# Optimization experiments

Measured on AMD Instinct MI355X. Metric: run time of the kernel, lower is better.

## Reference

```python
import jax, jax.numpy as jnp
import numpy as np

B, N, M, C, K = 4, 16384, 1024, 256, 32
RADIUS = 1.0
EPS = 1e-5


def _bn(x, g, b, axes):
    # training-mode batch norm over given axes; channel axis is 1
    m = jnp.mean(x, axes, keepdims=True)
    v = jnp.var(x, axes, keepdims=True)
    sh = [1] * x.ndim
    sh[1] = -1
    return (x - m) * jax.lax.rsqrt(v + EPS) * g.reshape(sh) + b.reshape(sh)


def setup_inputs() -> dict:
    key = jax.random.key(0)
    ks = jax.random.split(key, 10)
    d = {
        'ffps_xyz': jax.random.normal(ks[0], (B, M, 3), jnp.float32),
        'ffps_feature': jax.random.normal(ks[1], (B, C, M), jnp.float32),
        'backbone_xyz': jax.random.normal(ks[2], (B, N, 3), jnp.float32),
        'backbone_features': jax.random.normal(ks[3], (B, C, N), jnp.float32),
        # shift layer: Conv1d(256->128), Conv1d(128->3)
        'sw1': jax.random.normal(ks[4], (128, 256), jnp.float32) * 0.05,
        'sg1': jnp.ones((128,), jnp.float32), 'sb1': jnp.zeros((128,), jnp.float32),
        'sw2': jax.random.normal(ks[5], (3, 128), jnp.float32) * 0.05,
        'sg2': jnp.ones((3,), jnp.float32), 'sb2': jnp.zeros((3,), jnp.float32),
        # grouped MLP: Conv2d 1x1: 259->512->512->512
        'w1': jax.random.normal(ks[6], (512, C + 3), jnp.float32) * 0.05,
        'g1': jnp.ones((512,), jnp.float32), 'b1': jnp.zeros((512,), jnp.float32),
        'w2': jax.random.normal(ks[7], (512, 512), jnp.float32) * 0.05,
        'g2': jnp.ones((512,), jnp.float32), 'b2': jnp.zeros((512,), jnp.float32),
        'w3': jax.random.normal(ks[8], (512, 512), jnp.float32) * 0.05,
        'g3': jnp.ones((512,), jnp.float32), 'b3': jnp.zeros((512,), jnp.float32),
    }
    return d


def reference(ffps_xyz, ffps_feature, backbone_xyz, backbone_features,
              sw1, sg1, sb1, sw2, sg2, sb2,
              w1, g1, b1, w2, g2, b2, w3, g3, b3):
    # ---- shift layer: Conv1d(1x1)+BN1d+ReLU x2 -> (B,3,M) ----
    h = jnp.einsum('oc,bcm->bom', sw1, ffps_feature)
    h = jax.nn.relu(_bn(h, sg1, sb1, (0, 2)))
    h = jnp.einsum('oc,bcm->bom', sw2, h)
    shift = jax.nn.relu(_bn(h, sg2, sb2, (0, 2)))
    new_xyz = ffps_xyz + shift.transpose(0, 2, 1)  # (B,M,3)

    # ---- ball query: first K points within RADIUS, pad with first hit ----
    d2 = jnp.sum((new_xyz[:, :, None, :] - backbone_xyz[:, None, :, :]) ** 2, -1)  # (B,M,N)
    score = jnp.where(d2 < RADIUS * RADIUS, jnp.arange(N, dtype=jnp.int32), N)
    neg_vals, _ = jax.lax.top_k(-score, K)  # K smallest scores = first valid indices
    idx = -neg_vals  # (B,M,K)
    first = idx[..., :1]
    idx = jnp.where(idx == N, first, idx)
    idx = jnp.where(idx == N, 0, idx)  # query with no neighbors -> 0

    # ---- group: relative xyz concat features -> (B, 3+C, M, K) ----
    bidx = jnp.arange(B)[:, None, None]
    g_xyz = backbone_xyz[bidx, idx] - new_xyz[:, :, None, :]        # (B,M,K,3)
    g_feat = backbone_features.transpose(0, 2, 1)[bidx, idx]        # (B,M,K,C)
    g = jnp.concatenate([g_xyz, g_feat], -1).transpose(0, 3, 1, 2)  # (B,3+C,M,K)

    # ---- per-point MLP: Conv2d(1x1)+BN2d+ReLU x3 ----
    for w, gm, bt in ((w1, g1, b1), (w2, g2, b2), (w3, g3, b3)):
        g = jnp.einsum('oc,bcmk->bomk', w, g)
        g = jax.nn.relu(_bn(g, gm, bt, (0, 2, 3)))

    # ---- max-pool over neighbors, return (B, M, C_out) ----
    return jnp.max(g, axis=3).transpose(0, 2, 1)
```

## Files before the change

### kernel.cpp

```cpp
#include <hip/hip_runtime.h>
#include <hip/hip_bf16.h>
#include <hip/hip_fp16.h>

#define BB   4
#define NN   16384
#define MM   1024
#define CC   256
#define KK   32
#define O1   128
#define FF   512
#define LTOT (BB*MM*KK)
#define NSLOT 64
#define CH   16384
#define NCH2 (LTOT/CH)

typedef float f4 __attribute__((ext_vector_type(4)));
typedef short b8 __attribute__((ext_vector_type(8)));

__device__ __forceinline__ float bf2f(unsigned short u){
    return __uint_as_float(((unsigned int)u) << 16);
}
__device__ __forceinline__ float anyf(const void* p, size_t i, int f){
    if (f == 1) return bf2f(((const unsigned short*)p)[i]);
    if (f == 2) return __half2float(((const __half*)p)[i]);
    return ((const float*)p)[i];
}

__global__ void k_det(const unsigned short* __restrict__ u, int n, int* __restrict__ flag){
    if (threadIdx.x != 0 || blockIdx.x != 0) return;
    int W = n < 64 ? n : 64;
    bool allz = true;
    for (int k = 0; k < W; k++) if (u[k]){ allz = false; break; }
    if (allz){ *flag = 1; return; }
    if (u[0] == 0x3F80u){ *flag = 1; return; }
    if (u[0] == 0x3C00u){ *flag = 2; return; }
    if (W >= 2){
        unsigned int f0 = ((unsigned int)u[1] << 16) | u[0];
        if (__uint_as_float(f0) == 1.0f){ *flag = 0; return; }
    }
    int ce = 0, co = 0, ne = 0, no_ = 0;
    for (int k = 0; k < W; k++){
        unsigned short x = u[k];
        float v = fabsf(bf2f(x));
        int sane = (x == 0) || (v >= 0.0009765625f && v <= 64.f);
        if (k & 1){ no_++; co += sane; } else { ne++; ce += sane; }
    }
    if (ce * 4 >= ne * 3){ *flag = 1; return; }
    if (co * 4 >= no_ * 3 && ce * 5 < ne * 2){ *flag = 0; return; }
    *flag = 2;
}

__global__ __launch_bounds__(256) void k_cvtf(const void* __restrict__ src,
                                              float* __restrict__ dst, int n,
                                              const int* __restrict__ flag){
    int t = blockIdx.x * 256 + threadIdx.x;
    if (t >= n) return;
    dst[t] = anyf(src, t, *flag);
}

__global__ __launch_bounds__(256) void k_mlp1(const float* __restrict__ sw1,
                                              const float* __restrict__ feat,
                                              float* __restrict__ h1,
                                              float* __restrict__ stats1){
    int t = blockIdx.x * 256 + threadIdx.x;
    int m = t & (MM - 1);
    int o = (t >> 10) & (O1 - 1);
    int b = t >> 17;
    const float* fb = feat + (size_t)b * CC * MM + m;
    const float* w  = sw1 + o * CC;
    float acc = 0.f;
    #pragma unroll 8
    for (int c = 0; c < CC; c++) acc += w[c] * fb[(size_t)c * MM];
    h1[t] = acc;
    float s = acc, s2 = acc * acc;
    for (int off = 32; off; off >>= 1){ s += __shfl_down(s, off); s2 += __shfl_down(s2, off); }
    __shared__ float ls[8];
    int lane = threadIdx.x & 63, wid = threadIdx.x >> 6;
    if (lane == 0){ ls[wid] = s; ls[4 + wid] = s2; }
    __syncthreads();
    if (threadIdx.x == 0){
        atomicAdd(&stats1[2*o],   ls[0]+ls[1]+ls[2]+ls[3]);
        atomicAdd(&stats1[2*o+1], ls[4]+ls[5]+ls[6]+ls[7]);
    }
}

__global__ __launch_bounds__(256) void k_bn1mlp2(const float* __restrict__ h1,
                                                 const float* __restrict__ stats1,
                                                 const float* __restrict__ sg1,
                                                 const float* __restrict__ sb1,
                                                 const float* __restrict__ sw2,
                                                 float* __restrict__ h2,
                                                 float* __restrict__ stats2){
    __shared__ float sc[O1], bi[O1];
    int tid = threadIdx.x;
    if (tid < O1){
        const float invn = 1.f / (BB * MM);
        float mean = stats1[2*tid] * invn;
        float var  = fmaxf(stats1[2*tid+1] * invn - mean * mean, 0.f);
        float rs   = 1.f / sqrtf(var + 1e-5f);
        float s    = rs * sg1[tid];
        float b_   = sb1[tid] - mean * s;
        if (!isfinite(s) || !isfinite(b_)){ s = 1.f; b_ = 0.f; }
        sc[tid] = s; bi[tid] = b_;
    }
    __syncthreads();
    int t = blockIdx.x * 256 + tid;
    int m = t & (MM - 1);
    int r = t >> 10; int o2 = r % 3; int b = r / 3;
    const float* hb = h1 + (size_t)b * O1 * MM + m;
    const float* w  = sw2 + o2 * O1;
    float acc = 0.f;
    #pragma unroll 8
    for (int c = 0; c < O1; c++){
        float v = hb[(size_t)c * MM] * sc[c] + bi[c];
        v = v > 0.f ? v : 0.f;
        acc += w[c] * v;
    }
    h2[t] = acc;
    float s = acc, s2 = acc * acc;
    for (int off = 32; off; off >>= 1){ s += __shfl_down(s, off); s2 += __shfl_down(s2, off); }
    __shared__ float ls[8];
    int lane = tid & 63, wid = tid >> 6;
    if (lane == 0){ ls[wid] = s; ls[4 + wid] = s2; }
    __syncthreads();
    if (tid == 0){
        atomicAdd(&stats2[2*o2],   ls[0]+ls[1]+ls[2]+ls[3]);
        atomicAdd(&stats2[2*o2+1], ls[4]+ls[5]+ls[6]+ls[7]);
    }
}

__global__ void k_fin2(const float* __restrict__ stats2, const float* __restrict__ sg2,
                       const float* __restrict__ sb2, float* __restrict__ scb2){
    int t = threadIdx.x;
    if (t < 3){
        const float invn = 1.f / (BB * MM);
        float mean = stats2[2*t] * invn;
        float var  = fmaxf(stats2[2*t+1] * invn - mean * mean, 0.f);
        float rs   = 1.f / sqrtf(var + 1e-5f);
        float s    = rs * sg2[t];
        float b    = sb2[t] - mean * s;
        if (!isfinite(s) || !isfinite(b)){ s = 1.f; b = 0.f; }
        scb2[t] = s; scb2[4 + t] = b;
    }
}

__global__ __launch_bounds__(256) void k_ballq(const float* __restrict__ fxyz,
                                               const float* __restrict__ h2,
                                               const float* __restrict__ scb2,
                                               const float* __restrict__ bxyz,
                                               float* __restrict__ nxyz,
                                               int* __restrict__ idxbuf){
    int q    = blockIdx.x * 4 + (threadIdx.x >> 6);
    int lane = threadIdx.x & 63;
    int b = q >> 10, m = q & (MM - 1);
    float nx[3];
    #pragma unroll
    for (int c = 0; c < 3; c++){
        float v = h2[((size_t)b * 3 + c) * MM + m] * scb2[c] + scb2[4 + c];
        v = v > 0.f ? v : 0.f;
        nx[c] = fxyz[(size_t)q * 3 + c] + v;
    }
    if (lane == 0){
        nxyz[q*3+0] = nx[0]; nxyz[q*3+1] = nx[1]; nxyz[q*3+2] = nx[2];
    }
    const float* bx = bxyz + (size_t)b * NN * 3;
    int have = 0, firstj = 0;
    int* out = idxbuf + (size_t)q * KK;
    for (int j0 = 0; j0 < NN && have < KK; j0 += 64){
        int j = j0 + lane;
        float dx = bx[j*3+0] - nx[0];
        float dy = bx[j*3+1] - nx[1];
        float dz = bx[j*3+2] - nx[2];
        float d2 = dx*dx + dy*dy + dz*dz;
        bool pred = d2 < 1.0f;
        unsigned long long mask = __ballot(pred);
        if (mask){
            if (have == 0) firstj = j0 + (__ffsll((unsigned long long)mask) - 1);
            if (pred){
                int rank = __popcll(mask & ((1ull << lane) - 1ull));
                int pos = have + rank;
                if (pos < KK) out[pos] = j;
            }
            have += (int)__popcll(mask);
        }
    }
    if (have < KK){
        int fill = (have > 0) ? firstj : 0;
        for (int p = have + lane; p < KK; p += 64) out[p] = fill;
    }
}

__global__ __launch_bounds__(256) void k_xyzd(const int* __restrict__ idxbuf,
                                              const float* __restrict__ bxyz,
                                              const float* __restrict__ nxyz,
                                              int* __restrict__ idx2,
                                              float4* __restrict__ xyzd){
    int l = blockIdx.x * 256 + threadIdx.x;
    int b = l >> 15;
    int q = l >> 5;
    int j = idxbuf[l];
    idx2[l] = b * NN + j;
    const float* p = bxyz + ((size_t)b * NN + j) * 3;
    xyzd[l] = make_float4(p[0] - nxyz[q*3+0], p[1] - nxyz[q*3+1], p[2] - nxyz[q*3+2], 0.f);
}

__global__ __launch_bounds__(256) void k_transp(const void* __restrict__ bfv,
                                                const int* __restrict__ flag,
                                                float* __restrict__ ft){
    __shared__ float tile[32][33];
    int f = *flag;
    int bid = blockIdx.x;
    int nt = bid & 511;
    int ct = (bid >> 9) & 7;
    int b  = bid >> 12;
    int tx = threadIdx.x & 31, ty = threadIdx.x >> 5;
    size_t base = ((size_t)b * CC + ct * 32) * NN + nt * 32;
    #pragma unroll
    for (int r = 0; r < 32; r += 8)
        tile[ty + r][tx] = anyf(bfv, base + (size_t)(ty + r) * NN + tx, f);
    __syncthreads();
    float* dst = ft + ((size_t)b * NN + nt * 32) * CC + ct * 32;
    #pragma unroll
    for (int r = 0; r < 32; r += 8) dst[(size_t)(ty + r) * CC + tx] = tile[tx][ty + r];
}

__global__ void k_wprep(const float* __restrict__ w1,
                        unsigned short* __restrict__ w1h,
                        unsigned short* __restrict__ w1l,
                        float4* __restrict__ w1xp){
    int t = blockIdx.x * 256 + threadIdx.x;
    int o = t >> 8, c = t & 255;
    float f = w1[o * 259 + 3 + c];
    unsigned u = __float_as_uint(f);
    unsigned hh = u & 0xFFFF0000u;
    w1h[t] = (unsigned short)(hh >> 16);
    float f2 = f - __uint_as_float(hh);
    w1l[t] = (unsigned short)(__float_as_uint(f2) >> 16);
    if (t < 512) w1xp[t] = make_float4(w1[t*259], w1[t*259+1], w1[t*259+2], 0.f);
}

__global__ __launch_bounds__(256) void k_wsplit(const float* __restrict__ src,
                                                unsigned short* __restrict__ h,
                                                unsigned short* __restrict__ l, int n){
    int t = blockIdx.x * 256 + threadIdx.x;
    if (t >= n) return;
    float f = src[t];
    unsigned u = __float_as_uint(f);
    unsigned hh = u & 0xFFFF0000u;
    h[t] = (unsigned short)(hh >> 16);
    float f2 = f - __uint_as_float(hh);
    l[t] = (unsigned short)(__float_as_uint(f2) >> 16);
}

__device__ __forceinline__ void split4(float x, float y, float z_, float w_,
                                       unsigned &h0, unsigned &h1,
                                       unsigned &lo0, unsigned &lo1){
    unsigned ux = __float_as_uint(x), uy = __float_as_uint(y);
    unsigned uz = __float_as_uint(z_), uw = __float_as_uint(w_);
    unsigned hx = ux & 0xFFFF0000u, hy = uy & 0xFFFF0000u;
    unsigned hz = uz & 0xFFFF0000u, hw = uw & 0xFFFF0000u;
    h0 = (hx >> 16) | hy;
    h1 = (hz >> 16) | hw;
    float rx = x  - __uint_as_float(hx);
    float ry = y  - __uint_as_float(hy);
    float rz = z_ - __uint_as_float(hz);
    float rw = w_ - __uint_as_float(hw);
    lo0 = (__float_as_uint(rx) >> 16) | (__float_as_uint(ry) & 0xFFFF0000u);
    lo1 = (__float_as_uint(rz) >> 16) | (__float_as_uint(rw) & 0xFFFF0000u);
}

template<int XM, int OM>
__global__ __launch_bounds__(256) void k_gemm(const unsigned short* __restrict__ Ah,
                                              const unsigned short* __restrict__ Al,
                                              const float* __restrict__ X,
                                              int Cs,
                                              const float* __restrict__ scb,
                                              const int* __restrict__ idx2,
                                              const float4* __restrict__ xyzd,
                                              const float4* __restrict__ w1xp,
                                              int Lbase,
                                              float* __restrict__ Y,
                                              int Lwrite,
                                              float* __restrict__ y3mx,
                                              float* __restrict__ y3mn,
                                              double* __restrict__ stats){
    __shared__ short lds[16384];
    char* ldsb = (char*)lds;

    const int tid  = threadIdx.x;
    const int lane = tid & 63;
    const int w    = tid >> 6;
    const int wo   = (w >> 1) * 64;
    const int wl   = (w & 1) * 64;

    int bid = blockIdx.x;
    {
        int cpx = gridDim.x >> 3;
        bid = (bid & 7) * cpx + (bid >> 3);
    }
    const int o0 = (bid & 3) * 128;
    const int l0 = (bid >> 2) * 128;

    const int o_loc  = tid >> 3;
    const int q      = (tid & 7) >> 1;
    const int h      = tid & 1;
    const int colOff = q * 8 + h * 4;
    const int wbase  = ((o_loc >> 4) * 1024) + (((o_loc & 15) * 16) ^ (q << 5)) + (q << 8) + h * 8;
    const int roff   = (((lane & 15) * 16) ^ ((lane >> 4) << 5)) + ((lane >> 4) << 8);

    const unsigned short* Ahp = Ah + (size_t)(o0 + o_loc) * Cs + colOff;
    const unsigned short* Alp = Al + (size_t)(o0 + o_loc) * Cs + colOff;

    int   rI[4];
    float ddx[4], ddy[4], ddz[4];
    const float* Xp = nullptr;
    if (XM == 1){
        #pragma unroll
        for (int i = 0; i < 4; i++){
            int lg = Lbase + l0 + o_loc + 32 * i;
            rI[i] = idx2[lg];
            float4 dd = xyzd[lg];
            ddx[i] = dd.x; ddy[i] = dd.y; ddz[i] = dd.z;
        }
    } else {
        Xp = X + (size_t)(l0 + o_loc) * Cs + colOff;
    }

    f4 acc[4][4];
    #pragma unroll
    for (int i = 0; i < 4; i++)
        #pragma unroll
        for (int j = 0; j < 4; j++)
            acc[i][j] = f4{0.f, 0.f, 0.f, 0.f};

    uint2  rah[4], ral[4];
    float4 rx[4];
    #pragma unroll
    for (int i = 0; i < 4; i++){
        rah[i] = *(const uint2*)(Ahp + (size_t)(32 * i) * Cs);
        ral[i] = *(const uint2*)(Alp + (size_t)(32 * i) * Cs);
        if (XM == 1) rx[i] = *(const float4*)(X + (size_t)rI[i] * FF + colOff);
        else         rx[i] = *(const float4*)(Xp + (size_t)(32 * i) * Cs);
    }

    for (int c0 = 0; c0 < Cs; c0 += 32){
        unsigned xh0[4], xh1[4], xL0[4], xL1[4];
        float4 sc4, bi4;
        if (scb){
            sc4 = *(const float4*)(scb + c0 + colOff);
            bi4 = *(const float4*)(scb + Cs + c0 + colOff);
        }
        float4 wv0, wv1, wv2, wv3;
        if (XM == 1){
            wv0 = w1xp[c0 + colOff + 0];
            wv1 = w1xp[c0 + colOff + 1];
            wv2 = w1xp[c0 + colOff + 2];
            wv3 = w1xp[c0 + colOff + 3];
        }
        #pragma unroll
        for (int i = 0; i < 4; i++){
            float vx = rx[i].x, vy = rx[i].y, vz = rx[i].z, vw = rx[i].w;
            if (XM == 1){
                vx += ddx[i]*wv0.x + ddy[i]*wv0.y + ddz[i]*wv0.z;
                vy += ddx[i]*wv1.x + ddy[i]*wv1.y + ddz[i]*wv1.z;
                vz += ddx[i]*wv2.x + ddy[i]*wv2.y + ddz[i]*wv2.z;
                vw += ddx[i]*wv3.x + ddy[i]*wv3.y + ddz[i]*wv3.z;
            }
            if (scb){
                vx = fmaxf(vx * sc4.x + bi4.x, 0.f);
                vy = fmaxf(vy * sc4.y + bi4.y, 0.f);
                vz = fmaxf(vz * sc4.z + bi4.z, 0.f);
                vw = fmaxf(vw * sc4.w + bi4.w, 0.f);
            }
            split4(vx, vy, vz, vw, xh0[i], xh1[i], xL0[i], xL1[i]);
        }
        __syncthreads();
        #pragma unroll
        for (int i = 0; i < 4; i++){
            int off = wbase + i * 2048;
            *(uint2*)(ldsb + off)          = rah[i];
            *(uint2*)(ldsb + 8192  + off)  = ral[i];
            *(uint2*)(ldsb + 16384 + off)  = make_uint2(xh0[i], xh1[i]);
            *(uint2*)(ldsb + 24576 + off)  = make_uint2(xL0[i], xL1[i]);
        }
        __syncthreads();
        if (c0 + 32 < Cs){
            #pragma unroll
            for (int i = 0; i < 4; i++){
                rah[i] = *(const uint2*)(Ahp + (size_t)(32 * i) * Cs + (c0 + 32));
                ral[i] = *(const uint2*)(Alp + (size_t)(32 * i) * Cs + (c0 + 32));
                if (XM == 1) rx[i] = *(const float4*)(X + (size_t)rI[i] * FF + colOff + (c0 + 32));
                else         rx[i] = *(const float4*)(Xp + (size_t)(32 * i) * Cs + (c0 + 32));
            }
        }
        b8 bhf[4], blf[4];
        #pragma unroll
        for (int ni = 0; ni < 4; ni++){
            int f = (wl >> 4) + ni;
            bhf[ni] = *(const b8*)(ldsb + 16384 + f * 1024 + roff);
            blf[ni] = *(const b8*)(ldsb + 24576 + f * 1024 + roff);
        }
        #pragma unroll
        for (int mi = 0; mi < 4; mi++){
            int f = (wo >> 4) + mi;
            b8 ahf = *(const b8*)(ldsb + f * 1024 + roff);
            b8 alf = *(const b8*)(ldsb + 8192 + f * 1024 + roff);
            #pragma unroll
            for (int ni = 0; ni < 4; ni++){
                acc[mi][ni] = __builtin_amdgcn_mfma_f32_16x16x32_bf16(ahf, bhf[ni], acc[mi][ni], 0, 0, 0);
                acc[mi][ni] = __builtin_amdgcn_mfma_f32_16x16x32_bf16(ahf, blf[ni], acc[mi][ni], 0, 0, 0);
                acc[mi][ni] = __builtin_amdgcn_mfma_f32_16x16x32_bf16(alf, bhf[ni], acc[mi][ni], 0, 0, 0);
            }
        }
    }

    if (OM == 0){
        if (Y && (l0 + 128 <= Lwrite)){
            #pragma unroll
            for (int mi = 0; mi < 4; mi++){
                #pragma unroll
                for (int ni = 0; ni < 4; ni++){
                    int o = o0 + wo + mi * 16 + 4 * (lane >> 4);
                    int l = l0 + wl + ni * 16 + (lane & 15);
                    *(float4*)(Y + (size_t)l * FF + o) =
                        make_float4(acc[mi][ni][0], acc[mi][ni][1], acc[mi][ni][2], acc[mi][ni][3]);
                }
            }
        }
    }
    if (stats){
        int slot_s = blockIdx.x & (NSLOT - 1);
        double* sp = stats + (size_t)slot_s * FF * 2;
        #pragma unroll
        for (int mi = 0; mi < 4; mi++){
            float s1[4] = {0,0,0,0}, s2[4] = {0,0,0,0};
            #pragma unroll
            for (int ni = 0; ni < 4; ni++){
                #pragma unroll
                for (int r = 0; r < 4; r++){
                    float v = acc[mi][ni][r];
                    s1[r] += v; s2[r] += v * v;
                }
            }
            #pragma unroll
            for (int off = 8; off; off >>= 1){
                #pragma unroll
                for (int r = 0; r < 4; r++){
                    s1[r] += __shfl_down(s1[r], off, 16);
                    s2[r] += __shfl_down(s2[r], off, 16);
                }
            }
            if ((lane & 15) == 0){
                int o = o0 + wo + mi * 16 + 4 * (lane >> 4);
                #pragma unroll
                for (int r = 0; r < 4; r++){
                    atomicAdd(&sp[2 * (o + r)],     (double)s1[r]);
                    atomicAdd(&sp[2 * (o + r) + 1], (double)s2[r]);
                }
            }
        }
    }
    if (OM == 1){
        #pragma unroll
        for (int mi = 0; mi < 4; mi++){
            #pragma unroll
            for (int g = 0; g < 2; g++){
                float vmx[4], vmn[4];
                #pragma unroll
                for (int r = 0; r < 4; r++){
                    float a0 = acc[mi][2*g][r], a1 = acc[mi][2*g+1][r];
                    vmx[r] = fmaxf(a0, a1); vmn[r] = fminf(a0, a1);
                }
                #pragma unroll
                for (int off = 8; off; off >>= 1){
                    #pragma unroll
                    for (int r = 0; r < 4; r++){
                        vmx[r] = fmaxf(vmx[r], __shfl_down(vmx[r], off, 16));
                        vmn[r] = fminf(vmn[r], __shfl_down(vmn[r], off, 16));
                    }
                }
                if ((lane & 15) == 0){
                    int qg = (Lbase + l0 + wl) / 32 + g;
                    #pragma unroll
                    for (int r = 0; r < 4; r++){
                        int o = o0 + wo + mi * 16 + 4 * (lane >> 4) + r;
                        y3mx[(size_t)qg * FF + o] = vmx[r];
                        y3mn[(size_t)qg * FF + o] = vmn[r];
                    }
                }
            }
        }
    }
}

__global__ void k_finL(const double* __restrict__ stats, const float* __restrict__ g,
                       const float* __restrict__ bt, float* __restrict__ scb){
    int o = blockIdx.x * 256 + threadIdx.x;
    double s = 0.0, s2 = 0.0;
    for (int k = 0; k < NSLOT; k++){
        s  += stats[((size_t)k * FF + o) * 2];
        s2 += stats[((size_t)k * FF + o) * 2 + 1];
    }
    double mean = s / (double)LTOT;
    double var  = s2 / (double)LTOT - mean * mean;
    if (!(var > 0.0)) var = 0.0;
    double rs = 1.0 / sqrt(var + 1e-5);
    double sc = rs * (double)g[o];
    double bi = (double)bt[o] - mean * sc;
    float scf = (float)sc, bif = (float)bi;
    if (!isfinite(scf) || !isfinite(bif)){ scf = 1.f; bif = 0.f; }
    scb[o] = scf;
    scb[FF + o] = bif;
}

__global__ __launch_bounds__(256) void k_y1stats(const float* __restrict__ z,
                                                 const int* __restrict__ idx2,
                                                 const float4* __restrict__ xyzd,
                                                 const float4* __restrict__ w1xp,
                                                 double* __restrict__ stats){
    int tid = threadIdx.x, bid = blockIdx.x;
    int o1 = tid, o2 = tid + 256;
    float4 wa = w1xp[o1], wb = w1xp[o2];
    double s1a=0, s2a=0, s1b=0, s2b=0;
    for (int p = 0; p < LTOT/2048; p++){
        int l = bid + p * 2048;
        int r = idx2[l];
        float4 d = xyzd[l];
        const float* zr = z + (size_t)r * FF;
        float ya = zr[o1] + d.x*wa.x + d.y*wa.y + d.z*wa.z;
        float yb = zr[o2] + d.x*wb.x + d.y*wb.y + d.z*wb.z;
        s1a += ya; s2a += (double)ya*ya;
        s1b += yb; s2b += (double)yb*yb;
    }
    int slot = bid & (NSLOT - 1);
    double* sp = stats + (size_t)slot * FF * 2;
    atomicAdd(&sp[2*o1],   s1a); atomicAdd(&sp[2*o1+1], s2a);
    atomicAdd(&sp[2*o2],   s1b); atomicAdd(&sp[2*o2+1], s2b);
}

__global__ __launch_bounds__(256) void k_bn3max(const float* __restrict__ mx,
                                                const float* __restrict__ mn,
                                                const float* __restrict__ scb,
                                                float* __restrict__ out){
    int t = blockIdx.x * 256 + threadIdx.x;
    int o = t & (FF - 1);
    float sc = scb[o], bi = scb[FF + o];
    float v = sc >= 0.f ? mx[t] : mn[t];
    out[t] = fmaxf(sc * v + bi, 0.f);
}

__global__ __launch_bounds__(256) void k_diag(const float* __restrict__ ff,
                                              const float* __restrict__ w1f,
                                              const float* __restrict__ featT,
                                              const float* __restrict__ z,
                                              const float* __restrict__ xyzdf,
                                              const float* __restrict__ scb1,
                                              const float* __restrict__ scbL2,
                                              const float* __restrict__ scbL3,
                                              const float* __restrict__ y3,
                                              float* __restrict__ out){
    __shared__ float red[4];
    int tid = threadIdx.x;
    int bad = 0, isn = 0;
    const float* arr[9] = {ff, w1f, featT, z, xyzdf, scb1, scbL2, scbL3, y3};
    const int   len[9] = {4096, 4096, 8192, 8192, 4096, 1024, 1024, 1024, 8192};
    for (int k = 0; k < 9; k++){
        float s = 0.f;
        const float* a = arr[k];
        for (int i = tid; i < len[k]; i += 256) s += fabsf(a[i]);
        for (int off = 32; off; off >>= 1) s += __shfl_down(s, off);
        if ((tid & 63) == 0) red[tid >> 6] = s;
        __syncthreads();
        float t = red[0] + red[1] + red[2] + red[3];
        __syncthreads();
        if (bad == 0 && !(t > 1e-6f && t < 1e15f)){
            bad = k + 1;
            isn = isfinite(t) ? 0 : 1;
        }
    }
    if (tid == 0 && bad) out[0] = 512.f * bad + 256.f * isn;
}

extern "C" void kernel_launch(void* const* d_in, const int* in_sizes, int n_in,
                              void* d_out, int out_size, void* d_ws, size_t ws_size,
                              hipStream_t stream) {
    static const int NSZ[19] = {12288, 1048576, 196608, 16777216, 32768, 128, 128,
                                384, 3, 3, 132608, 512, 512, 262144, 512, 512,
                                262144, 512, 512};
    float* out = (float*)d_out;

    char* w = (char*)d_ws;
    size_t off = 0;
    auto take = [&](size_t bytes)->size_t{
        size_t r = off; off += (bytes + 255) & ~(size_t)255; return r;
    };
    size_t o_stats1  = take(256 * 4);
    size_t o_stats2  = take(8 * 4);
    size_t o_statsA  = take((size_t)NSLOT * FF * 2 * 8);
    size_t o_statsL2 = take((size_t)NSLOT * FF * 2 * 8);
    size_t o_statsL3 = take((size_t)NSLOT * FF * 2 * 8);
    size_t zero_end  = off;
    size_t o_flags   = take(19 * 4);
    size_t o_cv[19];
    for (int i = 0; i < 19; i++){
        if (i == 3){ o_cv[i] = 0; continue; }
        o_cv[i] = take((size_t)NSZ[i] * 4);
    }
    size_t o_scb2    = take(8 * 4);
    size_t o_scb1    = take(FF * 2 * 4);
    size_t o_scbL2   = take(FF * 2 * 4);
    size_t o_scbL3   = take(FF * 2 * 4);
    size_t o_h1      = take((size_t)BB * O1 * MM * 4);
    size_t o_h2      = take((size_t)BB * 3 * MM * 4);
    size_t o_nxyz    = take((size_t)BB * MM * 3 * 4);
    size_t o_idx     = take((size_t)LTOT * 4);
    size_t o_idx2    = take((size_t)LTOT * 4);
    size_t o_xyzd    = take((size_t)LTOT * 16);
    size_t o_w1h     = take((size_t)FF * CC * 2);
    size_t o_w1l     = take((size_t)FF * CC * 2);
    size_t o_w2h     = take((size_t)FF * FF * 2);
    size_t o_w2l     = take((size_t)FF * FF * 2);
    size_t o_w3h     = take((size_t)FF * FF * 2);
    size_t o_w3l     = take((size_t)FF * FF * 2);
    size_t o_w1xp    = take((size_t)FF * 16);
    size_t o_y3mx    = take((size_t)BB * MM * FF * 4);
    size_t o_y3mn    = take((size_t)BB * MM * FF * 4);
    size_t o_z       = take((size_t)BB * NN * FF * 4);
    size_t o_featT   = take((size_t)BB * NN * CC * 4);
    (void)n_in; (void)in_sizes; (void)out_size;

    const size_t chb = (size_t)CH * FF * 4;
    size_t avail = ws_size > o_featT ? ws_size - o_featT : 0;
    int S; bool full;
    if (avail >= (size_t)NCH2 * chb){ S = NCH2; full = true; }
    else {
        long s = (long)(avail / chb) - 1;
        if (s < 0) s = 0; if (s > NCH2 - 1) s = NCH2 - 1;
        S = (int)s; full = false;
    }
    const int Lwrite = S * CH;

    float*  stats1  = (float*) (w + o_stats1);
    float*  stats2  = (float*) (w + o_stats2);
    double* statsA  = (double*)(w + o_statsA);
    double* statsL2 = (double*)(w + o_statsL2);
    double* statsL3 = (double*)(w + o_statsL3);
    int*    flags   = (int*)   (w + o_flags);
    float*  scb2    = (float*) (w + o_scb2);
    float*  scb1    = (float*) (w + o_scb1);
    float*  scbL2   = (float*) (w + o_scbL2);
    float*  scbL3   = (float*) (w + o_scbL3);
    float*  h1      = (float*) (w + o_h1);
    float*  h2      = (float*) (w + o_h2);
    float*  nxyz    = (float*) (w + o_nxyz);
    int*    idxbuf  = (int*)   (w + o_idx);
    int*    idx2    = (int*)   (w + o_idx2);
    float4* xyzd    = (float4*)(w + o_xyzd);
    unsigned short* w1h = (unsigned short*)(w + o_w1h);
    unsigned short* w1l = (unsigned short*)(w + o_w1l);
    unsigned short* w2h = (unsigned short*)(w + o_w2h);
    unsigned short* w2l = (unsigned short*)(w + o_w2l);
    unsigned short* w3h = (unsigned short*)(w + o_w3h);
    unsigned short* w3l = (unsigned short*)(w + o_w3l);
    float4* w1xp    = (float4*)(w + o_w1xp);
    float*  y3mx    = (float*) (w + o_y3mx);
    float*  y3mn    = (float*) (w + o_y3mn);
    float*  z       = (float*) (w + o_z);
    float*  featT   = (float*) (w + o_featT);
    float*  t2scr   = featT;
    float*  t2store = full ? featT : featT + (size_t)CH * FF;

    hipMemsetAsync(w, 0, zero_end, stream);

    float* cv[19];
    for (int i = 0; i < 19; i++){
        k_det<<<1, 64, 0, stream>>>((const unsigned short*)d_in[i], NSZ[i], flags + i);
        if (i == 3){ cv[i] = nullptr; continue; }
        cv[i] = (float*)(w + o_cv[i]);
    }
    for (int i = 0; i < 19; i++){
        if (i == 3) continue;
        k_cvtf<<<(NSZ[i] + 255) / 256, 256, 0, stream>>>(d_in[i], cv[i], NSZ[i], flags + i);
    }
    float* fx = cv[0], *ffp = cv[1], *bx = cv[2];
    float* sw1f = cv[4], *sg1f = cv[5], *sb1f = cv[6];
    float* sw2f = cv[7], *sg2f = cv[8], *sb2f = cv[9];
    float* w1f = cv[10], *g1f = cv[11], *b1f = cv[12];
    float* w2f = cv[13], *g2f = cv[14], *b2f = cv[15];
    float* w3f = cv[16], *g3f = cv[17], *b3f = cv[18];

    k_mlp1   <<<2048, 256, 0, stream>>>(sw1f, ffp, h1, stats1);
    k_bn1mlp2<<<48,   256, 0, stream>>>(h1, stats1, sg1f, sb1f, sw2f, h2, stats2);
    k_fin2   <<<1,    64,  0, stream>>>(stats2, sg2f, sb2f, scb2);
    k_ballq  <<<BB*MM/4, 256, 0, stream>>>(fx, h2, scb2, bx, nxyz, idxbuf);
    k_xyzd   <<<LTOT/256, 256, 0, stream>>>(idxbuf, bx, nxyz, idx2, xyzd);
    k_transp <<<BB*(CC/32)*(NN/32), 256, 0, stream>>>(d_in[3], flags + 3, featT);
    k_wprep  <<<512, 256, 0, stream>>>(w1f, w1h, w1l, w1xp);
    k_wsplit <<<1024, 256, 0, stream>>>(w2f, w2h, w2l, FF*FF);
    k_wsplit <<<1024, 256, 0, stream>>>(w3f, w3h, w3l, FF*FF);

    k_gemm<0,0><<<4 * (BB*NN/128), 256, 0, stream>>>(w1h, w1l, featT, CC, nullptr,
            nullptr, nullptr, nullptr, 0, z, BB*NN, nullptr, nullptr, nullptr);

    k_y1stats<<<2048, 256, 0, stream>>>(z, idx2, xyzd, w1xp, statsA);
    k_finL  <<<2, 256, 0, stream>>>(statsA, g1f, b1f, scb1);

    const int GFULL = 4 * (LTOT/128);
    const int GCH   = 4 * (CH/128);

    k_gemm<1,0><<<GFULL, 256, 0, stream>>>(w2h, w2l, z, FF, scb1,
            idx2, xyzd, w1xp, 0, t2store, Lwrite, nullptr, nullptr, statsL2);
    k_finL <<<2, 256, 0, stream>>>(statsL2, g2f, b2f, scbL2);

    if (S > 0){
        k_gemm<0,1><<<S * GCH, 256, 0, stream>>>(w3h, w3l, t2store, FF, scbL2,
                nullptr, nullptr, nullptr, 0, nullptr, 0, y3mx, y3mn, statsL3);
    }
    for (int c = S; c < NCH2; c++){
        k_gemm<1,0><<<GCH, 256, 0, stream>>>(w2h, w2l, z, FF, scb1,
                idx2, xyzd, w1xp, c*CH, t2scr, CH, nullptr, nullptr, nullptr);
        k_gemm<0,1><<<GCH, 256, 0, stream>>>(w3h, w3l, t2scr, FF, scbL2,
                nullptr, nullptr, nullptr, c*CH, nullptr, 0, y3mx, y3mn, statsL3);
    }
    k_finL <<<2, 256, 0, stream>>>(statsL3, g3f, b3f, scbL3);

    k_bn3max<<<(BB*MM*FF)/256, 256, 0, stream>>>(y3mx, y3mn, scbL3, out);

    k_diag<<<1, 256, 0, stream>>>(ffp, w1f, t2scr, z, (const float*)xyzd,
                                  scb1, scbL2, scbL3, y3mx, out);
}
```

Baseline: 1.677 ms.

## Prepack weights into MFMA fragment layout and batch input conversion launches

Weights are pre-split into hi/lo bf16 and stored in MFMA fragment order, so each GEMM wave loads its A operands straight from global memory into registers. This drops the A tiles from LDS, halving shared memory per block and removing their LDS writes and reads. The next K-step's A fragments are prefetched into registers, which raises register pressure. Separately, 37 tiny per-input detect and convert launches are merged into two batched kernels to cut launch overhead.

```diff
diff --git a/kernel.cpp b/kernel.cpp
--- a/kernel.cpp
+++ b/kernel.cpp
@@ -17,6 +17,13 @@
 typedef float f4 __attribute__((ext_vector_type(4)));
 typedef short b8 __attribute__((ext_vector_type(8)));
 
+struct CvtA {
+    const void* src[19];
+    unsigned cum[20];
+    unsigned dstF[19];
+    int      nsz[19];
+};
+
 __device__ __forceinline__ float bf2f(unsigned short u){
     return __uint_as_float(((unsigned int)u) << 16);
 }
@@ -26,8 +33,12 @@
     return ((const float*)p)[i];
 }
 
-__global__ void k_det(const unsigned short* __restrict__ u, int n, int* __restrict__ flag){
-    if (threadIdx.x != 0 || blockIdx.x != 0) return;
+__global__ void k_det19(CvtA a, int* __restrict__ flags){
+    if (threadIdx.x != 0) return;
+    int i = blockIdx.x;
+    const unsigned short* u = (const unsigned short*)a.src[i];
+    int n = a.nsz[i];
+    int* flag = flags + i;
     int W = n < 64 ? n : 64;
     bool allz = true;
     for (int k = 0; k < W; k++) if (u[k]){ allz = false; break; }
@@ -50,12 +61,14 @@
     *flag = 2;
 }
 
-__global__ __launch_bounds__(256) void k_cvtf(const void* __restrict__ src,
-                                              float* __restrict__ dst, int n,
-                                              const int* __restrict__ flag){
-    int t = blockIdx.x * 256 + threadIdx.x;
-    if (t >= n) return;
-    dst[t] = anyf(src, t, *flag);
+__global__ __launch_bounds__(256) void k_cvt19(CvtA a, const int* __restrict__ flags,
+                                               float* __restrict__ base){
+    unsigned eb = blockIdx.x * 256u;
+    int i = 0;
+    while (eb >= a.cum[i+1]) i++;
+    unsigned tl = eb - a.cum[i] + threadIdx.x;
+    if ((int)tl >= a.nsz[i]) return;
+    base[a.dstF[i] + tl] = anyf(a.src[i], tl, flags[i]);
 }
 
 __global__ __launch_bounds__(256) void k_mlp1(const float* __restrict__ sw1,
@@ -224,32 +237,31 @@
     for (int r = 0; r < 32; r += 8) dst[(size_t)(ty + r) * CC + tx] = tile[tx][ty + r];
 }
 
-__global__ void k_wprep(const float* __restrict__ w1,
-                        unsigned short* __restrict__ w1h,
-                        unsigned short* __restrict__ w1l,
-                        float4* __restrict__ w1xp){
+__global__ __launch_bounds__(256) void k_wpack(const float* __restrict__ src,
+                                               int stride, int srcOff, int Cs,
+                                               unsigned short* __restrict__ hph,
+                                               unsigned short* __restrict__ hpl){
     int t = blockIdx.x * 256 + threadIdx.x;
-    int o = t >> 8, c = t & 255;
-    float f = w1[o * 259 + 3 + c];
+    if (t >= FF * Cs) return;
+    int nK = Cs >> 5;
+    int j  = t & 7;
+    int ln = (t >> 3) & 63;
+    int r  = t >> 9;
+    int ks = r % nK;
+    int of = r / nK;
+    int o = of * 16 + (ln & 15);
+    int c = ks * 32 + (ln >> 4) * 8 + ((j >> 2) << 2) + (j & 3);
+    float f = src[(size_t)o * stride + srcOff + c];
     unsigned u = __float_as_uint(f);
     unsigned hh = u & 0xFFFF0000u;
-    w1h[t] = (unsigned short)(hh >> 16);
+    hph[t] = (unsigned short)(hh >> 16);
     float f2 = f - __uint_as_float(hh);
-    w1l[t] = (unsigned short)(__float_as_uint(f2) >> 16);
-    if (t < 512) w1xp[t] = make_float4(w1[t*259], w1[t*259+1], w1[t*259+2], 0.f);
-}
-
-__global__ __launch_bounds__(256) void k_wsplit(const float* __restrict__ src,
-                                                unsigned short* __restrict__ h,
-                                                unsigned short* __restrict__ l, int n){
+    hpl[t] = (unsigned short)(__float_as_uint(f2) >> 16);
+}
+
+__global__ void k_w1xyz(const float* __restrict__ w1, float4* __restrict__ w1xp){
     int t = blockIdx.x * 256 + threadIdx.x;
-    if (t >= n) return;
-    float f = src[t];
-    unsigned u = __float_as_uint(f);
-    unsigned hh = u & 0xFFFF0000u;
-    h[t] = (unsigned short)(hh >> 16);
-    float f2 = f - __uint_as_float(hh);
-    l[t] = (unsigned short)(__float_as_uint(f2) >> 16);
+    if (t < FF) w1xp[t] = make_float4(w1[t*259], w1[t*259+1], w1[t*259+2], 0.f);
 }
 
 __device__ __forceinline__ void split4(float x, float y, float z_, float w_,
@@ -270,8 +282,8 @@
 }
 
 template<int XM, int OM>
-__global__ __launch_bounds__(256) void k_gemm(const unsigned short* __restrict__ Ah,
-                                              const unsigned short* __restrict__ Al,
+__global__ __launch_bounds__(256) void k_gemm(const unsigned short* __restrict__ Aph,
+                                              const unsigned short* __restrict__ Apl,
                                               const float* __restrict__ X,
                                               int Cs,
                                               const float* __restrict__ scb,
@@ -284,7 +296,7 @@
                                               float* __restrict__ y3mx,
                                               float* __restrict__ y3mn,
                                               double* __restrict__ stats){
-    __shared__ short lds[16384];
+    __shared__ short lds[8192];
     char* ldsb = (char*)lds;
 
     const int tid  = threadIdx.x;
@@ -308,8 +320,9 @@
     const int wbase  = ((o_loc >> 4) * 1024) + (((o_loc & 15) * 16) ^ (q << 5)) + (q << 8) + h * 8;
     const int roff   = (((lane & 15) * 16) ^ ((lane >> 4) << 5)) + ((lane >> 4) << 8);
 
-    const unsigned short* Ahp = Ah + (size_t)(o0 + o_loc) * Cs + colOff;
-    const unsigned short* Alp = Al + (size_t)(o0 + o_loc) * Cs + colOff;
+    const int nK    = Cs >> 5;
+    const int fbase = (o0 + wo) >> 4;
+    const int aLane = lane * 16;
 
     int   rI[4];
     float ddx[4], ddy[4], ddz[4];
@@ -333,14 +346,15 @@
         for (int j = 0; j < 4; j++)
             acc[i][j] = f4{0.f, 0.f, 0.f, 0.f};
 
-    uint2  rah[4], ral[4];
     float4 rx[4];
+    b8 ahf[4], alf[4];
     #pragma unroll
     for (int i = 0; i < 4; i++){
-        rah[i] = *(const uint2*)(Ahp + (size_t)(32 * i) * Cs);
-        ral[i] = *(const uint2*)(Alp + (size_t)(32 * i) * Cs);
         if (XM == 1) rx[i] = *(const float4*)(X + (size_t)rI[i] * FF + colOff);
         else         rx[i] = *(const float4*)(Xp + (size_t)(32 * i) * Cs);
+        int ab = ((fbase + i) * nK) << 10;
+        ahf[i] = *(const b8*)((const char*)Aph + ab + aLane);
+        alf[i] = *(const b8*)((const char*)Apl + ab + aLane);
     }
 
     for (int c0 = 0; c0 < Cs; c0 += 32){
@@ -378,39 +392,41 @@
         #pragma unroll
         for (int i = 0; i < 4; i++){
             int off = wbase + i * 2048;
-            *(uint2*)(ldsb + off)          = rah[i];
-            *(uint2*)(ldsb + 8192  + off)  = ral[i];
-            *(uint2*)(ldsb + 16384 + off)  = make_uint2(xh0[i], xh1[i]);
-            *(uint2*)(ldsb + 24576 + off)  = make_uint2(xL0[i], xL1[i]);
+            *(uint2*)(ldsb + off)         = make_uint2(xh0[i], xh1[i]);
+            *(uint2*)(ldsb + 8192 + off)  = make_uint2(xL0[i], xL1[i]);
         }
         __syncthreads();
+        b8 nah[4], nal[4];
         if (c0 + 32 < Cs){
+            int ks1 = (c0 >> 5) + 1;
             #pragma unroll
             for (int i = 0; i < 4; i++){
-                rah[i] = *(const uint2*)(Ahp + (size_t)(32 * i) * Cs + (c0 + 32));
-                ral[i] = *(const uint2*)(Alp + (size_t)(32 * i) * Cs + (c0 + 32));
                 if (XM == 1) rx[i] = *(const float4*)(X + (size_t)rI[i] * FF + colOff + (c0 + 32));
                 else         rx[i] = *(const float4*)(Xp + (size_t)(32 * i) * Cs + (c0 + 32));
+                int ab = (((fbase + i) * nK + ks1)) << 10;
+                nah[i] = *(const b8*)((const char*)Aph + ab + aLane);
+                nal[i] = *(const b8*)((const char*)Apl + ab + aLane);
             }
         }
         b8 bhf[4], blf[4];
         #pragma unroll
         for (int ni = 0; ni < 4; ni++){
             int f = (wl >> 4) + ni;
-            bhf[ni] = *(const b8*)(ldsb + 16384 + f * 1024 + roff);
-            blf[ni] = *(const b8*)(ldsb + 24576 + f * 1024 + roff);
+            bhf[ni] = *(const b8*)(ldsb + f * 1024 + roff);
+            blf[ni] = *(const b8*)(ldsb + 8192 + f * 1024 + roff);
         }
         #pragma unroll
         for (int mi = 0; mi < 4; mi++){
-            int f = (wo >> 4) + mi;
-            b8 ahf = *(const b8*)(ldsb + f * 1024 + roff);
-            b8 alf = *(const b8*)(ldsb + 8192 + f * 1024 + roff);
             #pragma unroll
             for (int ni = 0; ni < 4; ni++){
-                acc[mi][ni] = __builtin_amdgcn_mfma_f32_16x16x32_bf16(ahf, bhf[ni], acc[mi][ni], 0, 0, 0);
-                acc[mi][ni] = __builtin_amdgcn_mfma_f32_16x16x32_bf16(ahf, blf[ni], acc[mi][ni], 0, 0, 0);
-                acc[mi][ni] = __builtin_amdgcn_mfma_f32_16x16x32_bf16(alf, bhf[ni], acc[mi][ni], 0, 0, 0);
-            }
+                acc[mi][ni] = __builtin_amdgcn_mfma_f32_16x16x32_bf16(ahf[mi], bhf[ni], acc[mi][ni], 0, 0, 0);
+                acc[mi][ni] = __builtin_amdgcn_mfma_f32_16x16x32_bf16(ahf[mi], blf[ni], acc[mi][ni], 0, 0, 0);
+                acc[mi][ni] = __builtin_amdgcn_mfma_f32_16x16x32_bf16(alf[mi], bhf[ni], acc[mi][ni], 0, 0, 0);
+            }
+        }
+        if (c0 + 32 < Cs){
+            #pragma unroll
+            for (int i = 0; i < 4; i++){ ahf[i] = nah[i]; alf[i] = nal[i]; }
         }
     }
 
@@ -672,16 +688,29 @@
 
     hipMemsetAsync(w, 0, zero_end, stream);
 
+    CvtA ca;
+    unsigned cum = 0;
+    for (int i = 0; i < 19; i++){
+        ca.src[i]  = d_in[i];
+        ca.nsz[i]  = NSZ[i];
+        ca.dstF[i] = (unsigned)(o_cv[i] / 4);
+        ca.cum[i]  = cum;
+        if (i != 3) cum += (unsigned)((NSZ[i] + 255) & ~255);
+    }
+    ca.cum[19] = cum;
+    {
+        unsigned c2 = 0;
+        for (int i = 0; i < 19; i++){
+            ca.cum[i] = c2;
+            if (i != 3) c2 += (unsigned)((NSZ[i] + 255) & ~255);
+        }
+        ca.cum[19] = c2;
+    }
+    k_det19<<<19, 64, 0, stream>>>(ca, flags);
+    k_cvt19<<<ca.cum[19] / 256, 256, 0, stream>>>(ca, flags, (float*)w);
+
     float* cv[19];
-    for (int i = 0; i < 19; i++){
-        k_det<<<1, 64, 0, stream>>>((const unsigned short*)d_in[i], NSZ[i], flags + i);
-        if (i == 3){ cv[i] = nullptr; continue; }
-        cv[i] = (float*)(w + o_cv[i]);
-    }
-    for (int i = 0; i < 19; i++){
-        if (i == 3) continue;
-        k_cvtf<<<(NSZ[i] + 255) / 256, 256, 0, stream>>>(d_in[i], cv[i], NSZ[i], flags + i);
-    }
+    for (int i = 0; i < 19; i++) cv[i] = (i == 3) ? nullptr : (float*)(w + o_cv[i]);
     float* fx = cv[0], *ffp = cv[1], *bx = cv[2];
     float* sw1f = cv[4], *sg1f = cv[5], *sb1f = cv[6];
     float* sw2f = cv[7], *sg2f = cv[8], *sb2f = cv[9];
@@ -695,9 +724,10 @@
     k_ballq  <<<BB*MM/4, 256, 0, stream>>>(fx, h2, scb2, bx, nxyz, idxbuf);
     k_xyzd   <<<LTOT/256, 256, 0, stream>>>(idxbuf, bx, nxyz, idx2, xyzd);
     k_transp <<<BB*(CC/32)*(NN/32), 256, 0, stream>>>(d_in[3], flags + 3, featT);
-    k_wprep  <<<512, 256, 0, stream>>>(w1f, w1h, w1l, w1xp);
-    k_wsplit <<<1024, 256, 0, stream>>>(w2f, w2h, w2l, FF*FF);
-    k_wsplit <<<1024, 256, 0, stream>>>(w3f, w3h, w3l, FF*FF);
+    k_wpack  <<<(FF*CC)/256, 256, 0, stream>>>(w1f, 259, 3, CC, w1h, w1l);
+    k_wpack  <<<(FF*FF)/256, 256, 0, stream>>>(w2f, FF, 0, FF, w2h, w2l);
+    k_wpack  <<<(FF*FF)/256, 256, 0, stream>>>(w3f, FF, 0, FF, w3h, w3l);
+    k_w1xyz  <<<2, 256, 0, stream>>>(w1f, w1xp);
 
     k_gemm<0,0><<<4 * (BB*NN/128), 256, 0, stream>>>(w1h, w1l, featT, CC, nullptr,
             nullptr, nullptr, nullptr, 0, z, BB*NN, nullptr, nullptr, nullptr);
```

After: 1.497 ms. 1.12x faster.
